# Kernel tuning notes

Measured on AMD Instinct MI355X. Metric: run time of the kernel, lower is better.

Reference implementation:

```python
import jax, jax.numpy as jnp
import numpy as np

G_ZERO_INIT = 32.0  # g initialized to log2(g0^2 - g0)


def setup_inputs() -> dict:
    key = jax.random.key(0)
    k1, k2, k3 = jax.random.split(key, 3)
    B, L, D = 64, 16384, 64
    query = jax.random.normal(k1, (B, 1, D), dtype=jnp.float32)
    keys = jax.random.normal(k2, (B, L, D), dtype=jnp.float32)
    values = jax.random.normal(k3, (B, L, 1), dtype=jnp.float32)
    g = jnp.asarray(np.log2(G_ZERO_INIT**2 - G_ZERO_INIT), dtype=jnp.float32)
    return {"query": query, "keys": keys, "values": values, "g": g, "k": 256}


def reference(query, keys, values, g, k):
    # cosine similarity between query (B,1,D) and keys (B,L,D) -> (B,L)
    qn = query / jnp.linalg.norm(query, axis=-1, keepdims=True)
    kn = keys / jnp.linalg.norm(keys, axis=-1, keepdims=True)
    similarity = jnp.einsum("bqd,bld->bl", qn, kn) * g  # (B, L)
    # top-k select + batched gather of values
    top_sim, idx = jax.lax.top_k(similarity, k)          # (B, k) each
    values_sel = jnp.take_along_axis(values, idx[:, :, None], axis=1)  # (B, k, 1)
    weights = jax.nn.softmax(top_sim, axis=-1)           # (B, k)
    return values_sel, weights
```

## Files before the change

kernel.cpp:

```cpp
#include <hip/hip_runtime.h>
#include <math.h>

#define BATCH 64
#define LSEQ  16384
#define DIM   64
#define KSEL  256
#define CHUNK 2048
#define NCHUNK (LSEQ / CHUNK)
#define NCAND (NCHUNK * KSEL)

__global__ __launch_bounds__(256) void sim_kernel(
    const float* __restrict__ q,
    const float* __restrict__ keys,
    const float* __restrict__ gp,
    double* __restrict__ sims)
{
    const int b     = blockIdx.x >> 6;
    const int chunk = blockIdx.x & 63;
    const int t  = threadIdx.x;
    const int j  = t & 15;
    const int rl = t >> 4;

    const float4* q4 = reinterpret_cast<const float4*>(q) + b * 16;
    float4 qv = q4[j];
    const double qx = qv.x, qy = qv.y, qz = qv.z, qw = qv.w;
    double qss = qx*qx + qy*qy + qz*qz + qw*qw;
    #pragma unroll
    for (int m = 1; m < 16; m <<= 1) qss += __shfl_xor(qss, m);
    const double scale = (double)gp[0] / sqrt(qss);

    __shared__ double local[256];
    const float4* k4 = reinterpret_cast<const float4*>(keys) + (size_t)b * LSEQ * 16;
    const int row_base = chunk * 256;

    for (int it = 0; it < 16; ++it) {
        const int row = row_base + it * 16 + rl;
        float4 kv = k4[row * 16 + j];
        const double kx = kv.x, ky = kv.y, kz = kv.z, kw = kv.w;
        double dot = qx*kx + qy*ky + qz*kz + qw*kw;
        double kss = kx*kx + ky*ky + kz*kz + kw*kw;
        #pragma unroll
        for (int m = 1; m < 16; m <<= 1) {
            dot += __shfl_xor(dot, m);
            kss += __shfl_xor(kss, m);
        }
        if (j == 0) local[it * 16 + rl] = scale * dot / sqrt(kss);
    }
    __syncthreads();
    sims[(size_t)b * LSEQ + row_base + t] = local[t];
}

__device__ __forceinline__ unsigned long long f64_sortable(double v) {
    unsigned long long u = (unsigned long long)__double_as_longlong(v);
    return (u >> 63) ? ~u : (u | 0x8000000000000000ull);
}
__device__ __forceinline__ double sortable_f64(unsigned long long k) {
    unsigned long long u = (k & 0x8000000000000000ull)
                         ? (k ^ 0x8000000000000000ull) : ~k;
    return __longlong_as_double((long long)u);
}

__global__ __launch_bounds__(256) void stage1_kernel(
    const double* __restrict__ sims,
    ulonglong2* __restrict__ cand)
{
    const int b     = blockIdx.x >> 3;
    const int chunk = blockIdx.x & 7;
    const int t     = threadIdx.x;
    const int base  = chunk * CHUNK;
    const double* s = sims + (size_t)b * LSEQ + base;

    __shared__ unsigned long long items[CHUNK];
    __shared__ unsigned lo[CHUNK];

    #pragma unroll
    for (int it = 0; it < CHUNK / 256; ++it) {
        int lidx = it * 256 + t;
        unsigned long long key = f64_sortable(s[lidx]);
        items[lidx] = (key & 0xFFFFFFFF00000000ull) |
                      (unsigned long long)(0xFFFFFFFFu - (unsigned)lidx);
        lo[lidx] = (unsigned)key;
    }

    for (int size = 2; size <= CHUNK; size <<= 1) {
        for (int stride = size >> 1; stride > 0; stride >>= 1) {
            __syncthreads();
            #pragma unroll
            for (int r = 0; r < CHUNK / 512; ++r) {
                int tt = r * 256 + t;
                int i  = ((tt & ~(stride - 1)) << 1) | (tt & (stride - 1));
                int jj = i + stride;
                bool up = ((i & size) == 0);
                unsigned long long a = items[i], c = items[jj];
                if ((a > c) == up) { items[i] = c; items[jj] = a; }
            }
        }
    }
    __syncthreads();

    unsigned long long item = items[CHUNK - 1 - t];
    unsigned lidx = 0xFFFFFFFFu - (unsigned)item;
    unsigned long long fullkey = (item & 0xFFFFFFFF00000000ull) |
                                 (unsigned long long)lo[lidx];
    cand[((size_t)b * NCHUNK + chunk) * KSEL + t] =
        make_ulonglong2(fullkey, (unsigned long long)(base + lidx));
}

__global__ __launch_bounds__(256) void stage2_kernel(
    const ulonglong2* __restrict__ cand,
    const float* __restrict__ values,
    float* __restrict__ out)
{
    const int b = blockIdx.x;
    const int t = threadIdx.x;
    const ulonglong2* c = cand + (size_t)b * NCAND;

    __shared__ ulonglong2 arr[NCAND];

    #pragma unroll
    for (int it = 0; it < NCAND / 256; ++it)
        arr[it * 256 + t] = c[it * 256 + t];

    for (int size = 2; size <= NCAND; size <<= 1) {
        for (int stride = size >> 1; stride > 0; stride >>= 1) {
            __syncthreads();
            #pragma unroll
            for (int r = 0; r < NCAND / 512; ++r) {
                int tt = r * 256 + t;
                int i  = ((tt & ~(stride - 1)) << 1) | (tt & (stride - 1));
                int jj = i + stride;
                bool up = ((i & size) == 0);
                ulonglong2 a = arr[i], cc = arr[jj];
                bool agt = (a.x > cc.x) || (a.x == cc.x && a.y < cc.y);
                if (agt == up) { arr[i] = cc; arr[jj] = a; }
            }
        }
    }
    __syncthreads();

    ulonglong2 v = arr[NCAND - 1 - t];
    unsigned idx = (unsigned)v.y;
    double sv = sortable_f64(v.x);
    double fm = sortable_f64(arr[NCAND - 1].x);

    double e = exp(sv - fm);
    double esum = e;
    #pragma unroll
    for (int m = 1; m < 64; m <<= 1) esum += __shfl_xor(esum, m);
    __shared__ double wsum[4];
    if ((t & 63) == 0) wsum[t >> 6] = esum;
    __syncthreads();
    const double tot = wsum[0] + wsum[1] + wsum[2] + wsum[3];

    out[b * KSEL + t]                = values[(size_t)b * LSEQ + idx];
    out[BATCH * KSEL + b * KSEL + t] = (float)(e / tot);
}

extern "C" void kernel_launch(void* const* d_in, const int* in_sizes, int n_in,
                              void* d_out, int out_size, void* d_ws, size_t ws_size,
                              hipStream_t stream)
{
    const float* q      = (const float*)d_in[0];
    const float* keys   = (const float*)d_in[1];
    const float* values = (const float*)d_in[2];
    const float* g      = (const float*)d_in[3];
    float* out   = (float*)d_out;

    double* sims     = (double*)d_ws;
    ulonglong2* cand = (ulonglong2*)((char*)d_ws + (size_t)BATCH * LSEQ * 8);

    sim_kernel<<<dim3(BATCH * (LSEQ / 256)), dim3(256), 0, stream>>>(q, keys, g, sims);
    stage1_kernel<<<dim3(BATCH * NCHUNK), dim3(256), 0, stream>>>(sims, cand);
    stage2_kernel<<<dim3(BATCH), dim3(256), 0, stream>>>(cand, values, out);
}
```

Before: 436.9 us.

## Replace full bitonic sorts with sort-256 runs plus top-k bitonic merge-prune

Stage 1 now uses 1024-element chunks. It sorts 256-element runs and then repeatedly merges pairs of runs, keeping only the larger 256 from each pair via a bitonic max-split. Full keys are recovered by reloading the sim values, so the separate lo array is gone. Stage 2 likewise replaces the full sort of all candidates with a pairwise merge-prune tree down to 256. This cuts the sorting work and the number of barriers per block, at the cost of more stage-1 blocks and a packed key that truncates the low 11 mantissa bits, which could change tie ordering among nearly equal similarities.

```diff
diff --git a/kernel.cpp b/kernel.cpp
--- a/kernel.cpp
+++ b/kernel.cpp
@@ -5,7 +5,8 @@
 #define LSEQ  16384
 #define DIM   64
 #define KSEL  256
-#define CHUNK 2048
+#define CHUNK 1024
+#define NRUNS (CHUNK / 256)
 #define NCHUNK (LSEQ / CHUNK)
 #define NCAND (NCHUNK * KSEL)
 
@@ -59,51 +60,99 @@
                          ? (k ^ 0x8000000000000000ull) : ~k;
     return __longlong_as_double((long long)u);
 }
+__device__ __forceinline__ bool rank_gt(ulonglong2 a, ulonglong2 b) {
+    return (a.x > b.x) || (a.x == b.x && a.y < b.y);
+}
 
 __global__ __launch_bounds__(256) void stage1_kernel(
     const double* __restrict__ sims,
     ulonglong2* __restrict__ cand)
 {
-    const int b     = blockIdx.x >> 3;
-    const int chunk = blockIdx.x & 7;
+    const int b     = blockIdx.x >> 4;
+    const int chunk = blockIdx.x & 15;
     const int t     = threadIdx.x;
     const int base  = chunk * CHUNK;
     const double* s = sims + (size_t)b * LSEQ + base;
 
     __shared__ unsigned long long items[CHUNK];
-    __shared__ unsigned lo[CHUNK];
-
-    #pragma unroll
-    for (int it = 0; it < CHUNK / 256; ++it) {
-        int lidx = it * 256 + t;
+    __shared__ ulonglong2 cand2[KSEL];
+
+    #pragma unroll
+    for (int r = 0; r < CHUNK / 256; ++r) {
+        int lidx = r * 256 + t;
         unsigned long long key = f64_sortable(s[lidx]);
-        items[lidx] = (key & 0xFFFFFFFF00000000ull) |
-                      (unsigned long long)(0xFFFFFFFFu - (unsigned)lidx);
-        lo[lidx] = (unsigned)key;
-    }
-
-    for (int size = 2; size <= CHUNK; size <<= 1) {
+        items[lidx] = (key & ~0x7FFull) | (unsigned long long)(0x7FF - lidx);
+    }
+
+    for (int size = 2; size <= 256; size <<= 1) {
         for (int stride = size >> 1; stride > 0; stride >>= 1) {
             __syncthreads();
             #pragma unroll
             for (int r = 0; r < CHUNK / 512; ++r) {
                 int tt = r * 256 + t;
-                int i  = ((tt & ~(stride - 1)) << 1) | (tt & (stride - 1));
-                int jj = i + stride;
+                int i = ((tt & ~(stride - 1)) << 1) | (tt & (stride - 1));
+                bool up = (size == 256) ? true : ((i & size) == 0);
+                unsigned long long a = items[i], c = items[i + stride];
+                if ((a > c) == up) { items[i] = c; items[i + stride] = a; }
+            }
+        }
+    }
+
+    for (int nr = NRUNS; nr > 1; nr >>= 1) {
+        const int nout = (nr >> 1) * 256;
+        __syncthreads();
+        unsigned long long keep[2];
+        #pragma unroll
+        for (int c = 0; c < 2; ++c) {
+            int lane = c * 256 + t;
+            if (lane < nout) {
+                int j = lane >> 8, i = lane & 255;
+                unsigned long long a = items[(2 * j) * 256 + i];
+                unsigned long long bb = items[(2 * j) * 256 + 511 - i];
+                keep[c] = a > bb ? a : bb;
+            }
+        }
+        __syncthreads();
+        #pragma unroll
+        for (int c = 0; c < 2; ++c) {
+            int lane = c * 256 + t;
+            if (lane < nout) items[lane] = keep[c];
+        }
+        for (int stride = 128; stride > 0; stride >>= 1) {
+            __syncthreads();
+            #pragma unroll
+            for (int c = 0; c < 1; ++c) {
+                int lane = t;
+                if (lane < (nout >> 1)) {
+                    int seg = lane >> 7, loc = lane & 127;
+                    int i = seg * 256 + (((loc & ~(stride - 1)) << 1) | (loc & (stride - 1)));
+                    unsigned long long a = items[i], cc = items[i + stride];
+                    if (a > cc) { items[i] = cc; items[i + stride] = a; }
+                }
+            }
+        }
+    }
+    __syncthreads();
+
+    {
+        unsigned long long item = items[t];
+        int lidx = 0x7FF - (int)(item & 0x7FF);
+        cand2[t] = make_ulonglong2(f64_sortable(s[lidx]),
+                                   (unsigned long long)(base + lidx));
+    }
+    for (int size = 2; size <= 256; size <<= 1) {
+        for (int stride = size >> 1; stride > 0; stride >>= 1) {
+            __syncthreads();
+            if (t < 128) {
+                int i = ((t & ~(stride - 1)) << 1) | (t & (stride - 1));
                 bool up = ((i & size) == 0);
-                unsigned long long a = items[i], c = items[jj];
-                if ((a > c) == up) { items[i] = c; items[jj] = a; }
-            }
-        }
-    }
-    __syncthreads();
-
-    unsigned long long item = items[CHUNK - 1 - t];
-    unsigned lidx = 0xFFFFFFFFu - (unsigned)item;
-    unsigned long long fullkey = (item & 0xFFFFFFFF00000000ull) |
-                                 (unsigned long long)lo[lidx];
-    cand[((size_t)b * NCHUNK + chunk) * KSEL + t] =
-        make_ulonglong2(fullkey, (unsigned long long)(base + lidx));
+                ulonglong2 a = cand2[i], c = cand2[i + stride];
+                if (rank_gt(a, c) == up) { cand2[i] = c; cand2[i + stride] = a; }
+            }
+        }
+    }
+    __syncthreads();
+    cand[((size_t)(b * NCHUNK + chunk)) * KSEL + t] = cand2[t];
 }
 
 __global__ __launch_bounds__(256) void stage2_kernel(
@@ -113,35 +162,52 @@
 {
     const int b = blockIdx.x;
     const int t = threadIdx.x;
-    const ulonglong2* c = cand + (size_t)b * NCAND;
-
     __shared__ ulonglong2 arr[NCAND];
 
     #pragma unroll
-    for (int it = 0; it < NCAND / 256; ++it)
-        arr[it * 256 + t] = c[it * 256 + t];
-
-    for (int size = 2; size <= NCAND; size <<= 1) {
-        for (int stride = size >> 1; stride > 0; stride >>= 1) {
+    for (int r = 0; r < NCAND / 256; ++r)
+        arr[r * 256 + t] = cand[(size_t)b * NCAND + r * 256 + t];
+
+    for (int nr = NCHUNK; nr > 1; nr >>= 1) {
+        const int nout = (nr >> 1) * 256;
+        __syncthreads();
+        ulonglong2 keep[8];
+        #pragma unroll
+        for (int c = 0; c < 8; ++c) {
+            int lane = c * 256 + t;
+            if (lane < nout) {
+                int j = lane >> 8, i = lane & 255;
+                ulonglong2 a  = arr[(2 * j) * 256 + i];
+                ulonglong2 bb = arr[(2 * j) * 256 + 511 - i];
+                keep[c] = rank_gt(a, bb) ? a : bb;
+            }
+        }
+        __syncthreads();
+        #pragma unroll
+        for (int c = 0; c < 8; ++c) {
+            int lane = c * 256 + t;
+            if (lane < nout) arr[lane] = keep[c];
+        }
+        for (int stride = 128; stride > 0; stride >>= 1) {
             __syncthreads();
             #pragma unroll
-            for (int r = 0; r < NCAND / 512; ++r) {
-                int tt = r * 256 + t;
-                int i  = ((tt & ~(stride - 1)) << 1) | (tt & (stride - 1));
-                int jj = i + stride;
-                bool up = ((i & size) == 0);
-                ulonglong2 a = arr[i], cc = arr[jj];
-                bool agt = (a.x > cc.x) || (a.x == cc.x && a.y < cc.y);
-                if (agt == up) { arr[i] = cc; arr[jj] = a; }
-            }
-        }
-    }
-    __syncthreads();
-
-    ulonglong2 v = arr[NCAND - 1 - t];
+            for (int c = 0; c < 4; ++c) {
+                int lane = c * 256 + t;
+                if (lane < (nout >> 1)) {
+                    int seg = lane >> 7, loc = lane & 127;
+                    int i = seg * 256 + (((loc & ~(stride - 1)) << 1) | (loc & (stride - 1)));
+                    ulonglong2 a = arr[i], cc = arr[i + stride];
+                    if (rank_gt(a, cc)) { arr[i] = cc; arr[i + stride] = a; }
+                }
+            }
+        }
+    }
+    __syncthreads();
+
+    ulonglong2 v = arr[255 - t];
     unsigned idx = (unsigned)v.y;
     double sv = sortable_f64(v.x);
-    double fm = sortable_f64(arr[NCAND - 1].x);
+    double fm = sortable_f64(arr[255].x);
 
     double e = exp(sv - fm);
     double esum = e;
```

Result: faster. 419.5 us (-4.0%).
